# Performance work log

Measured on AMD Instinct MI355X. Metric: run time of the kernel, lower is better.

The kernel has to match this reference:

```python
import jax, jax.numpy as jnp
import numpy as np

N_EMBED = 2048
N_HEAD = 2
HEAD_SIZE = N_EMBED // N_HEAD  # 1024; mask constraint requires T <= HEAD_SIZE


def setup_inputs() -> dict:
    key = jax.random.key(0)
    ks = jax.random.split(key, 9)
    B, T, C, H, D = 32, 1024, N_EMBED, N_HEAD, HEAD_SIZE
    s = 1.0 / np.sqrt(C)
    x = jax.random.normal(ks[0], (B, T, C), dtype=jnp.float32)
    # torch Linear convention: weight (out_features, in_features), y = x @ W.T + b
    Wq = jax.random.normal(ks[1], (H, D, C), dtype=jnp.float32) * s
    Wk = jax.random.normal(ks[2], (H, D, C), dtype=jnp.float32) * s
    Wv = jax.random.normal(ks[3], (H, D, C), dtype=jnp.float32) * s
    bq = jax.random.normal(ks[4], (H, D), dtype=jnp.float32) * 0.01
    bk = jax.random.normal(ks[5], (H, D), dtype=jnp.float32) * 0.01
    bv = jax.random.normal(ks[6], (H, D), dtype=jnp.float32) * 0.01
    Wo = jax.random.normal(ks[7], (C, H * D), dtype=jnp.float32) * s  # no bias
    return {"x": x, "Wq": Wq, "bq": bq, "Wk": Wk, "bk": bk, "Wv": Wv, "bv": bv, "Wo": Wo}


def reference(x, Wq, bq, Wk, bk, Wv, bv, Wo):
    B, T, C = x.shape
    # per-head projections, batched over heads: (B,T,C) x (H,D,C) -> (B,H,T,D)
    q = jnp.einsum('btc,hdc->bhtd', x, Wq) + bq[None, :, None, :]
    k = jnp.einsum('btc,hdc->bhtd', x, Wk) + bk[None, :, None, :]
    v = jnp.einsum('btc,hdc->bhtd', x, Wv) + bv[None, :, None, :]
    # NOTE: original scales by x.shape[-1]**-0.5 == n_embed**-0.5 (not head_size)
    scale = jnp.asarray(C, x.dtype) ** -0.5
    wei = jnp.einsum('bhtd,bhsd->bhts', q, k) * scale  # (B,H,T,T)
    causal = jnp.tril(jnp.ones((T, T), dtype=bool))
    wei = jnp.where(causal[None, None], wei, -jnp.inf)
    wei = jax.nn.softmax(wei, axis=-1)
    out = jnp.einsum('bhts,bhsd->bhtd', wei, v)  # (B,H,T,D)
    # concat heads along last dim: (B,T,H*D)
    out = out.transpose(0, 2, 1, 3).reshape(B, T, -1)
    return out @ Wo.T  # (B,T,C)
```

## Files before the change

kernel.cpp:

```cpp
#include <hip/hip_runtime.h>
#include <hip/hip_bf16.h>
#include <stdint.h>

typedef __bf16 bf16_t;
typedef __bf16 bf16x8 __attribute__((ext_vector_type(8)));
typedef float f32x4 __attribute__((ext_vector_type(4)));

#define AS1(p) ((const __attribute__((address_space(1))) void*)(uintptr_t)(p))
#define AS3(p) ((__attribute__((address_space(3))) void*)(uintptr_t)(p))

__device__ __forceinline__ void gload16(const bf16_t* g, bf16_t* l) {
  __builtin_amdgcn_global_load_lds(AS1(g), AS3(l), 16, 0, 0);
}

#define BAR()    { __builtin_amdgcn_s_barrier(); __builtin_amdgcn_sched_barrier(0); }
#define VMCNT0() { asm volatile("s_waitcnt vmcnt(0)" ::: "memory"); __builtin_amdgcn_sched_barrier(0); }
#define LGKM0()  { asm volatile("s_waitcnt lgkmcnt(0)" ::: "memory"); __builtin_amdgcn_sched_barrier(0); }

__device__ __forceinline__ void gemm256(const bf16_t* __restrict__ A, int lda,
                                        const bf16_t* __restrict__ B, int ldb,
                                        int nt, f32x4 acc[8][4], bf16_t* lds) {
  const int t = (int)threadIdx.x;
  const int lane = t & 63, w = t >> 6;
  const int wr = w >> 2, wc = w & 3;
  const int fr = lane & 15, fq = lane >> 4;
  char* ldsb = (char*)lds;

  const int o = t * 16;
  const int s = o ^ (((t >> 3) & 7) << 4);
  const int r0 = s >> 6, q0 = (s >> 4) & 3;
  const bf16_t* gA0 = A + (size_t)r0 * lda + q0 * 8;
  const bf16_t* gA1 = gA0 + (size_t)128 * lda;
  const bf16_t* gB0 = B + (size_t)r0 * ldb + q0 * 8;
  const bf16_t* gB1 = gB0 + (size_t)128 * ldb;

  const int x = ((fr >> 1) & 7) << 4;
  const int abase = wr * 8192 + ((fr * 64 + fq * 16) ^ x);
  const int bbase = wc * 4096 + ((fr * 64 + fq * 16) ^ x);

  bf16x8 af[4], bvv[4];

#define STAGE_A(cb, kh, kof) \
  gload16(gA0 + (kof) + (kh) * 32, lds + (cb) * 32768 + (kh) * 8192 + t * 8); \
  gload16(gA1 + (kof) + (kh) * 32, lds + (cb) * 32768 + (kh) * 8192 + 4096 + t * 8);
#define STAGE_B(cb, kh, kof) \
  gload16(gB0 + (kof) + (kh) * 32, lds + (cb) * 32768 + 16384 + (kh) * 8192 + t * 8); \
  gload16(gB1 + (kof) + (kh) * 32, lds + (cb) * 32768 + 16384 + (kh) * 8192 + 4096 + t * 8);
#define DS_LOAD(cb, kh, qm) \
  { const char* ap = ldsb + (cb) * 65536 + (kh) * 16384 + abase + (qm) * 4096; \
    const char* bp = ldsb + (cb) * 65536 + 32768 + (kh) * 16384 + bbase; \
    _Pragma("unroll") for (int i = 0; i < 4; ++i) af[i] = *(const bf16x8*)(ap + i * 1024); \
    _Pragma("unroll") for (int n = 0; n < 4; ++n) bvv[n] = *(const bf16x8*)(bp + n * 1024); }
#define MFMA16(qm) \
  { __builtin_amdgcn_s_setprio(1); \
    _Pragma("unroll") for (int i = 0; i < 4; ++i) \
      _Pragma("unroll") for (int n = 0; n < 4; ++n) \
        acc[(qm) * 4 + i][n] = __builtin_amdgcn_mfma_f32_16x16x32_bf16(af[i], bvv[n], acc[(qm) * 4 + i][n], 0, 0, 0); \
    __builtin_amdgcn_s_setprio(0); }

  STAGE_A(0, 0, 0) STAGE_B(0, 0, 0) STAGE_A(0, 1, 0) STAGE_B(0, 1, 0)
  VMCNT0() BAR()

  int kof = 64;
  for (int tt = 0; tt < nt - 1; ++tt, kof += 64) {
    const int cb = tt & 1;
    DS_LOAD(cb, 0, 0) STAGE_A(cb ^ 1, 0, kof) STAGE_A(cb ^ 1, 1, kof) LGKM0() MFMA16(0)
    DS_LOAD(cb, 0, 1) STAGE_B(cb ^ 1, 0, kof) STAGE_B(cb ^ 1, 1, kof) LGKM0() MFMA16(1)
    DS_LOAD(cb, 1, 0) LGKM0() MFMA16(0)
    DS_LOAD(cb, 1, 1) LGKM0() MFMA16(1)
    VMCNT0() BAR()
  }
  {
    const int cb = (nt - 1) & 1;
    DS_LOAD(cb, 0, 0) LGKM0() MFMA16(0)
    DS_LOAD(cb, 0, 1) LGKM0() MFMA16(1)
    DS_LOAD(cb, 1, 0) LGKM0() MFMA16(0)
    DS_LOAD(cb, 1, 1) LGKM0() MFMA16(1)
  }
#undef STAGE_A
#undef STAGE_B
#undef DS_LOAD
#undef MFMA16
}

#define EPI_VARS \
  const int t = (int)threadIdx.x; \
  const int lane = t & 63, w = t >> 6; \
  const int wr = w >> 2, wc = w & 3; \
  const int fr = lane & 15, fq = lane >> 4;

#define ZERO8x4(acc) \
  _Pragma("unroll") for (int _i = 0; _i < 8; ++_i) \
  _Pragma("unroll") for (int _j = 0; _j < 4; ++_j) { f32x4 _z = {0.f,0.f,0.f,0.f}; acc[_i][_j] = _z; }

__global__ void k_cvt(const float* __restrict__ s, bf16_t* __restrict__ d, long n8) {
  long i = (long)blockIdx.x * blockDim.x + threadIdx.x;
  long st = (long)gridDim.x * blockDim.x;
  for (; i < n8; i += st) {
    const float4* sp = (const float4*)(s + i * 8);
    float4 a = sp[0], b = sp[1];
    bf16x8 v;
    v[0] = (__bf16)a.x; v[1] = (__bf16)a.y; v[2] = (__bf16)a.z; v[3] = (__bf16)a.w;
    v[4] = (__bf16)b.x; v[5] = (__bf16)b.y; v[6] = (__bf16)b.z; v[7] = (__bf16)b.w;
    *(bf16x8*)(d + i * 8) = v;
  }
}

__global__ void k_fill(float* o, float v, long n) {
  long i = (long)blockIdx.x * blockDim.x + threadIdx.x;
  long st = (long)gridDim.x * blockDim.x;
  for (; i < n; i += st) o[i] = v;
}

__global__ __launch_bounds__(512, 2) void k_qkv256(
    const bf16_t* __restrict__ xb, const bf16_t* __restrict__ Wb,
    const float* __restrict__ bq, const float* __restrict__ bk, const float* __restrict__ bv,
    bf16_t* __restrict__ Q, bf16_t* __restrict__ K, bf16_t* __restrict__ Vt) {
  __shared__ __align__(16) bf16_t lds[65536];
  int bid = (int)blockIdx.x;
  int id = (bid & 7) * 384 + (bid >> 3);
  EPI_VARS
  f32x4 acc[8][4];
  ZERO8x4(acc)

  bool vmode = id >= 2048;
  int mt = 0, ntile = 0, tok = 0, wm = 0;
  const bf16_t *Ap, *Bp;
  if (!vmode) {
    mt = id & 127; ntile = id >> 7;
    Ap = xb + (size_t)mt * 256 * 2048;
    Bp = Wb + (size_t)ntile * 256 * 2048;
  } else {
    int vb = id - 2048;
    tok = vb & 127; wm = vb >> 7;
    Ap = Wb + (size_t)(16 + wm) * 256 * 2048;
    Bp = xb + (size_t)tok * 256 * 2048;
  }
  gemm256(Ap, 2048, Bp, 2048, 32, acc, lds);

  if (!vmode) {
    int sel = ntile >> 3;
    const float* bias = sel ? bk : bq;
    bf16_t* dst = sel ? K : Q;
    int cbase = (ntile & 7) * 256 + wc * 64;
#pragma unroll
    for (int ni = 0; ni < 4; ++ni) {
      int c2 = cbase + ni * 16 + fr;
      int h = c2 >> 10, d = c2 & 1023;
      float bb = bias[c2];
#pragma unroll
      for (int mi = 0; mi < 8; ++mi) {
        f32x4 a = acc[mi][ni];
#pragma unroll
        for (int r = 0; r < 4; ++r) {
          int m = mt * 256 + wr * 128 + mi * 16 + fq * 4 + r;
          int b = m >> 10, tk = m & 1023;
          dst[(((size_t)(b * 2 + h) << 10) + tk) * 1024 + d] = (bf16_t)(a[r] + bb);
        }
      }
    }
  } else {
#pragma unroll
    for (int mi = 0; mi < 8; ++mi) {
#pragma unroll
      for (int r = 0; r < 4; ++r) {
        int gd = wm * 256 + wr * 128 + mi * 16 + fq * 4 + r;
        int h = gd >> 10, d = gd & 1023;
        float bb = bv[gd];
#pragma unroll
        for (int ni = 0; ni < 4; ++ni) {
          int m = tok * 256 + wc * 64 + ni * 16 + fr;
          int b = m >> 10, tk = m & 1023;
          Vt[(((size_t)(b * 2 + h) << 10) + d) * 1024 + tk] = (bf16_t)(acc[mi][ni][r] + bb);
        }
      }
    }
  }
}

__global__ __launch_bounds__(512, 2) void k_s256(const bf16_t* __restrict__ Q,
                                                 const bf16_t* __restrict__ K,
                                                 float* __restrict__ S, int pbase) {
  __shared__ __align__(16) bf16_t lds[65536];
  int id = (int)blockIdx.x;
  int pc = id / 10, rem = id % 10;
  int ti = 0;
  while (rem > ti) { rem -= ti + 1; ++ti; }
  int tj = rem;
  size_t p = (size_t)(pbase + pc);
  EPI_VARS
  f32x4 acc[8][4];
  ZERO8x4(acc)
  gemm256(Q + (p << 20) + (size_t)ti * 256 * 1024, 1024,
          K + (p << 20) + (size_t)tj * 256 * 1024, 1024, 16, acc, lds);
  float* Sp = S + ((size_t)pc << 20);
  const float scale = 0.022097086912079608f;
#pragma unroll
  for (int mi = 0; mi < 8; ++mi)
#pragma unroll
    for (int ni = 0; ni < 4; ++ni) {
      int col = tj * 256 + wc * 64 + ni * 16 + fr;
      f32x4 a = acc[mi][ni];
#pragma unroll
      for (int r = 0; r < 4; ++r) {
        int row = ti * 256 + wr * 128 + mi * 16 + fq * 4 + r;
        Sp[((size_t)row << 10) + col] = a[r] * scale;
      }
    }
}

__global__ __launch_bounds__(256) void k_softmax(const float* __restrict__ S,
                                                 bf16_t* __restrict__ P) {
  int bid = blockIdx.x;
  int pc = bid >> 10, row = bid & 1023;
  const float* s = S + ((size_t)pc << 20) + ((size_t)row << 10);
  bf16_t* p = P + ((size_t)pc << 20) + ((size_t)row << 10);
  int cend = ((row >> 8) + 1) << 8;
  int t = threadIdx.x;
  __shared__ float red[8];
  float x[4];
  float mx = -1e30f;
#pragma unroll
  for (int j = 0; j < 4; ++j) {
    int c = t + 256 * j;
    x[j] = (c <= row) ? s[c] : -1e30f;
    mx = fmaxf(mx, x[j]);
  }
  for (int o = 32; o > 0; o >>= 1) mx = fmaxf(mx, __shfl_xor(mx, o));
  if (!(t & 63)) red[t >> 6] = mx;
  __syncthreads();
  mx = fmaxf(fmaxf(red[0], red[1]), fmaxf(red[2], red[3]));
  float e[4];
  float sum = 0.f;
#pragma unroll
  for (int j = 0; j < 4; ++j) {
    e[j] = (x[j] > -1e29f) ? __expf(x[j] - mx) : 0.f;
    sum += e[j];
  }
  for (int o = 32; o > 0; o >>= 1) sum += __shfl_xor(sum, o);
  if (!(t & 63)) red[4 + (t >> 6)] = sum;
  __syncthreads();
  sum = red[4] + red[5] + red[6] + red[7];
  float inv = 1.f / sum;
#pragma unroll
  for (int j = 0; j < 4; ++j) {
    int c = t + 256 * j;
    if (c < cend) p[c] = (bf16_t)(e[j] * inv);
  }
}

__global__ __launch_bounds__(512, 2) void k_pv256(const bf16_t* __restrict__ P,
                                                  const bf16_t* __restrict__ Vt,
                                                  bf16_t* __restrict__ O, int pbase) {
  __shared__ __align__(16) bf16_t lds[65536];
  int id = (int)blockIdx.x;
  int pc = id >> 4, rem = id & 15;
  int ti = rem >> 2, dj = rem & 3;
  size_t p = (size_t)(pbase + pc);
  EPI_VARS
  f32x4 acc[8][4];
  ZERO8x4(acc)
  gemm256(P + ((size_t)pc << 20) + (size_t)ti * 256 * 1024, 1024,
          Vt + (p << 20) + (size_t)dj * 256 * 1024, 1024, (ti + 1) * 4, acc, lds);
  int b = (int)(p >> 1), h = (int)(p & 1);
#pragma unroll
  for (int mi = 0; mi < 8; ++mi)
#pragma unroll
    for (int ni = 0; ni < 4; ++ni) {
      int dcol = dj * 256 + wc * 64 + ni * 16 + fr;
      f32x4 a = acc[mi][ni];
#pragma unroll
      for (int r = 0; r < 4; ++r) {
        int tk = ti * 256 + wr * 128 + mi * 16 + fq * 4 + r;
        O[(((size_t)b << 10) + tk) * 2048 + (h << 10) + dcol] = (bf16_t)a[r];
      }
    }
}

__global__ __launch_bounds__(512, 2) void k_out256(const bf16_t* __restrict__ O,
                                                   const bf16_t* __restrict__ W,
                                                   float* __restrict__ out) {
  __shared__ __align__(16) bf16_t lds[65536];
  int bid = (int)blockIdx.x;
  int id = (bid & 7) * 128 + (bid >> 3);
  int mt = id & 127, ntile = id >> 7;
  EPI_VARS
  f32x4 acc[8][4];
  ZERO8x4(acc)
  gemm256(O + (size_t)mt * 256 * 2048, 2048, W + (size_t)ntile * 256 * 2048, 2048, 32, acc, lds);
#pragma unroll
  for (int mi = 0; mi < 8; ++mi)
#pragma unroll
    for (int ni = 0; ni < 4; ++ni) {
      int col = ntile * 256 + wc * 64 + ni * 16 + fr;
      f32x4 a = acc[mi][ni];
#pragma unroll
      for (int r = 0; r < 4; ++r) {
        int row = mt * 256 + wr * 128 + mi * 16 + fq * 4 + r;
        out[(size_t)row * 2048 + col] = a[r];
      }
    }
}

extern "C" void kernel_launch(void* const* d_in, const int* in_sizes, int n_in,
                              void* d_out, int out_size, void* d_ws, size_t ws_size,
                              hipStream_t stream) {
  const float* x  = (const float*)d_in[0];
  const float* Wq = (const float*)d_in[1];
  const float* bq = (const float*)d_in[2];
  const float* Wk = (const float*)d_in[3];
  const float* bk = (const float*)d_in[4];
  const float* Wv = (const float*)d_in[5];
  const float* bv = (const float*)d_in[6];
  const float* Wo = (const float*)d_in[7];
  float* out = (float*)d_out;

  const size_t MiB = 1ull << 20;
  char* w = (char*)d_ws;
  bf16_t* xb    = (bf16_t*)w;
  bf16_t* Ob    = xb;
  bf16_t* Qb    = (bf16_t*)(w + 128 * MiB);
  bf16_t* Kb    = (bf16_t*)(w + 256 * MiB);
  bf16_t* Vt    = (bf16_t*)(w + 384 * MiB);
  bf16_t* Wqkvb = (bf16_t*)(w + 512 * MiB);
  bf16_t* Wob   = (bf16_t*)(w + 536 * MiB);
  float*  Sc    = (float*)(w + 544 * MiB);

  size_t rem = ws_size > 544 * MiB ? ws_size - 544 * MiB : 0;
  int NP = (int)(rem / (6 * MiB));
  if (NP > 64) NP = 64;
  if (NP < 1) {
    k_fill<<<2048, 256, 0, stream>>>(out, (float)(ws_size >> 20), (long)out_size);
    return;
  }
  bf16_t* Pc = (bf16_t*)(w + 544 * MiB + (size_t)NP * 4 * MiB);

  k_cvt<<<2048, 256, 0, stream>>>(x, xb, 8388608L);
  k_cvt<<<1024, 256, 0, stream>>>(Wq, Wqkvb, 524288L);
  k_cvt<<<1024, 256, 0, stream>>>(Wk, Wqkvb + 4194304, 524288L);
  k_cvt<<<1024, 256, 0, stream>>>(Wv, Wqkvb + 8388608, 524288L);
  k_cvt<<<1024, 256, 0, stream>>>(Wo, Wob, 524288L);

  k_qkv256<<<3072, 512, 0, stream>>>(xb, Wqkvb, bq, bk, bv, Qb, Kb, Vt);

  for (int base = 0; base < 64; base += NP) {
    int np = (64 - base) < NP ? (64 - base) : NP;
    k_s256<<<np * 10, 512, 0, stream>>>(Qb, Kb, Sc, base);
    k_softmax<<<np * 1024, 256, 0, stream>>>(Sc, Pc);
    k_pv256<<<np * 16, 512, 0, stream>>>(Pc, Vt, Ob, base);
  }

  k_out256<<<1024, 512, 0, stream>>>(Ob, Wob, out);
}
```

Before: 1.515 ms.

## Restructure GEMM pipeline with partial waits, store scores in bf16, wave-per-row softmax

The shared GEMM main loop now interleaves LDS reads and global-to-LDS staging per k-half, using partial vmcnt/lgkmcnt waits and two A-fragment register sets so MFMAs overlap outstanding loads. The score matrix is written in bf16 instead of fp32, halving score traffic and letting more head-pairs fit per chunk. Softmax becomes one wavefront per row with vectorized 16-byte loads and stores, removing the shared-memory reductions and block barriers. The changes lower score precision before softmax and rely on the finer-grained wait counts being correct.

New measurement: 1.475 ms. 2.6% less time.

```diff
diff --git a/kernel.cpp b/kernel.cpp
--- a/kernel.cpp
+++ b/kernel.cpp
@@ -13,9 +13,10 @@
   __builtin_amdgcn_global_load_lds(AS1(g), AS3(l), 16, 0, 0);
 }
 
-#define BAR()    { __builtin_amdgcn_s_barrier(); __builtin_amdgcn_sched_barrier(0); }
-#define VMCNT0() { asm volatile("s_waitcnt vmcnt(0)" ::: "memory"); __builtin_amdgcn_sched_barrier(0); }
-#define LGKM0()  { asm volatile("s_waitcnt lgkmcnt(0)" ::: "memory"); __builtin_amdgcn_sched_barrier(0); }
+#define SB()      __builtin_amdgcn_sched_barrier(0);
+#define BAR()     { __builtin_amdgcn_sched_barrier(0); __builtin_amdgcn_s_barrier(); __builtin_amdgcn_sched_barrier(0); }
+#define VMCNT(n)  { asm volatile("s_waitcnt vmcnt(" #n ")" ::: "memory"); __builtin_amdgcn_sched_barrier(0); }
+#define LGKM(n)   { asm volatile("s_waitcnt lgkmcnt(" #n ")" ::: "memory"); __builtin_amdgcn_sched_barrier(0); }
 
 __device__ __forceinline__ void gemm256(const bf16_t* __restrict__ A, int lda,
                                         const bf16_t* __restrict__ B, int ldb,
@@ -26,60 +27,77 @@
   const int fr = lane & 15, fq = lane >> 4;
   char* ldsb = (char*)lds;
 
-  const int o = t * 16;
-  const int s = o ^ (((t >> 3) & 7) << 4);
-  const int r0 = s >> 6, q0 = (s >> 4) & 3;
+  const int s0 = (t * 16) ^ (((t >> 3) & 7) << 4);
+  const int r0 = s0 >> 6, q0 = (s0 >> 4) & 3;
   const bf16_t* gA0 = A + (size_t)r0 * lda + q0 * 8;
   const bf16_t* gA1 = gA0 + (size_t)128 * lda;
   const bf16_t* gB0 = B + (size_t)r0 * ldb + q0 * 8;
   const bf16_t* gB1 = gB0 + (size_t)128 * ldb;
 
-  const int x = ((fr >> 1) & 7) << 4;
-  const int abase = wr * 8192 + ((fr * 64 + fq * 16) ^ x);
-  const int bbase = wc * 4096 + ((fr * 64 + fq * 16) ^ x);
-
-  bf16x8 af[4], bvv[4];
-
-#define STAGE_A(cb, kh, kof) \
-  gload16(gA0 + (kof) + (kh) * 32, lds + (cb) * 32768 + (kh) * 8192 + t * 8); \
-  gload16(gA1 + (kof) + (kh) * 32, lds + (cb) * 32768 + (kh) * 8192 + 4096 + t * 8);
-#define STAGE_B(cb, kh, kof) \
-  gload16(gB0 + (kof) + (kh) * 32, lds + (cb) * 32768 + 16384 + (kh) * 8192 + t * 8); \
-  gload16(gB1 + (kof) + (kh) * 32, lds + (cb) * 32768 + 16384 + (kh) * 8192 + 4096 + t * 8);
-#define DS_LOAD(cb, kh, qm) \
-  { const char* ap = ldsb + (cb) * 65536 + (kh) * 16384 + abase + (qm) * 4096; \
-    const char* bp = ldsb + (cb) * 65536 + 32768 + (kh) * 16384 + bbase; \
-    _Pragma("unroll") for (int i = 0; i < 4; ++i) af[i] = *(const bf16x8*)(ap + i * 1024); \
-    _Pragma("unroll") for (int n = 0; n < 4; ++n) bvv[n] = *(const bf16x8*)(bp + n * 1024); }
-#define MFMA16(qm) \
-  { __builtin_amdgcn_s_setprio(1); \
+  const int swz = (fr * 64 + fq * 16) ^ (((fr >> 1) & 7) << 4);
+  const int abase = wr * 8192 + swz;
+  const int bbase = 32768 + wc * 4096 + swz;
+
+  bf16x8 bb[4], aa0[4], aa1[4];
+
+#define STAGE_A(cb, kh, kof) { \
+    bf16_t* _d = lds + (cb) * 32768 + (kh) * 8192; \
+    gload16(gA0 + (kof) + (kh) * 32, _d + t * 8); \
+    gload16(gA1 + (kof) + (kh) * 32, _d + 4096 + t * 8); \
+  } SB()
+#define STAGE_B(cb, kh, kof) { \
+    bf16_t* _d = lds + (cb) * 32768 + 16384 + (kh) * 8192; \
+    gload16(gB0 + (kof) + (kh) * 32, _d + t * 8); \
+    gload16(gB1 + (kof) + (kh) * 32, _d + 4096 + t * 8); \
+  } SB()
+#define READ_B(cb, kh) { \
+    const char* _b = ldsb + (cb) * 65536 + (kh) * 16384 + bbase; \
+    _Pragma("unroll") for (int n = 0; n < 4; ++n) bb[n] = *(const bf16x8*)(_b + n * 1024); }
+#define READ_A(cb, kh, qm, dst) { \
+    const char* _a = ldsb + (cb) * 65536 + (kh) * 16384 + abase + (qm) * 4096; \
+    _Pragma("unroll") for (int i = 0; i < 4; ++i) dst[i] = *(const bf16x8*)(_a + i * 1024); }
+#define MFMA16(dst, qm) { \
+    __builtin_amdgcn_s_setprio(1); \
     _Pragma("unroll") for (int i = 0; i < 4; ++i) \
       _Pragma("unroll") for (int n = 0; n < 4; ++n) \
-        acc[(qm) * 4 + i][n] = __builtin_amdgcn_mfma_f32_16x16x32_bf16(af[i], bvv[n], acc[(qm) * 4 + i][n], 0, 0, 0); \
+        acc[(qm) * 4 + i][n] = __builtin_amdgcn_mfma_f32_16x16x32_bf16(dst[i], bb[n], acc[(qm) * 4 + i][n], 0, 0, 0); \
     __builtin_amdgcn_s_setprio(0); }
 
   STAGE_A(0, 0, 0) STAGE_B(0, 0, 0) STAGE_A(0, 1, 0) STAGE_B(0, 1, 0)
-  VMCNT0() BAR()
 
   int kof = 64;
   for (int tt = 0; tt < nt - 1; ++tt, kof += 64) {
     const int cb = tt & 1;
-    DS_LOAD(cb, 0, 0) STAGE_A(cb ^ 1, 0, kof) STAGE_A(cb ^ 1, 1, kof) LGKM0() MFMA16(0)
-    DS_LOAD(cb, 0, 1) STAGE_B(cb ^ 1, 0, kof) STAGE_B(cb ^ 1, 1, kof) LGKM0() MFMA16(1)
-    DS_LOAD(cb, 1, 0) LGKM0() MFMA16(0)
-    DS_LOAD(cb, 1, 1) LGKM0() MFMA16(1)
-    VMCNT0() BAR()
+    VMCNT(4) BAR()
+    READ_B(cb, 0) READ_A(cb, 0, 0, aa0)
+    STAGE_A(cb ^ 1, 0, kof)
+    READ_A(cb, 0, 1, aa1)
+    STAGE_B(cb ^ 1, 0, kof)
+    LGKM(4) MFMA16(aa0, 0)
+    LGKM(0) MFMA16(aa1, 1)
+    VMCNT(4) BAR()
+    READ_B(cb, 1) READ_A(cb, 1, 0, aa0)
+    STAGE_A(cb ^ 1, 1, kof)
+    READ_A(cb, 1, 1, aa1)
+    STAGE_B(cb ^ 1, 1, kof)
+    LGKM(4) MFMA16(aa0, 0)
+    LGKM(0) MFMA16(aa1, 1)
   }
   {
     const int cb = (nt - 1) & 1;
-    DS_LOAD(cb, 0, 0) LGKM0() MFMA16(0)
-    DS_LOAD(cb, 0, 1) LGKM0() MFMA16(1)
-    DS_LOAD(cb, 1, 0) LGKM0() MFMA16(0)
-    DS_LOAD(cb, 1, 1) LGKM0() MFMA16(1)
+    VMCNT(4) BAR()
+    READ_B(cb, 0) READ_A(cb, 0, 0, aa0) READ_A(cb, 0, 1, aa1)
+    LGKM(4) MFMA16(aa0, 0)
+    LGKM(0) MFMA16(aa1, 1)
+    VMCNT(0) BAR()
+    READ_B(cb, 1) READ_A(cb, 1, 0, aa0) READ_A(cb, 1, 1, aa1)
+    LGKM(4) MFMA16(aa0, 0)
+    LGKM(0) MFMA16(aa1, 1)
   }
 #undef STAGE_A
 #undef STAGE_B
-#undef DS_LOAD
+#undef READ_B
+#undef READ_A
 #undef MFMA16
 }
 
@@ -165,13 +183,13 @@
 #pragma unroll
       for (int r = 0; r < 4; ++r) {
         int gd = wm * 256 + wr * 128 + mi * 16 + fq * 4 + r;
-        int h = gd >> 10, d = gd & 1023;
+        int h = gd >> 10, dd = gd & 1023;
         float bb = bv[gd];
 #pragma unroll
         for (int ni = 0; ni < 4; ++ni) {
           int m = tok * 256 + wc * 64 + ni * 16 + fr;
           int b = m >> 10, tk = m & 1023;
-          Vt[(((size_t)(b * 2 + h) << 10) + d) * 1024 + tk] = (bf16_t)(acc[mi][ni][r] + bb);
+          Vt[(((size_t)(b * 2 + h) << 10) + dd) * 1024 + tk] = (bf16_t)(acc[mi][ni][r] + bb);
         }
       }
     }
@@ -180,7 +198,7 @@
 
 __global__ __launch_bounds__(512, 2) void k_s256(const bf16_t* __restrict__ Q,
                                                  const bf16_t* __restrict__ K,
-                                                 float* __restrict__ S, int pbase) {
+                                                 bf16_t* __restrict__ S, int pbase) {
   __shared__ __align__(16) bf16_t lds[65536];
   int id = (int)blockIdx.x;
   int pc = id / 10, rem = id % 10;
@@ -193,7 +211,7 @@
   ZERO8x4(acc)
   gemm256(Q + (p << 20) + (size_t)ti * 256 * 1024, 1024,
           K + (p << 20) + (size_t)tj * 256 * 1024, 1024, 16, acc, lds);
-  float* Sp = S + ((size_t)pc << 20);
+  bf16_t* Sp = S + ((size_t)pc << 20);
   const float scale = 0.022097086912079608f;
 #pragma unroll
   for (int mi = 0; mi < 8; ++mi)
@@ -204,49 +222,47 @@
 #pragma unroll
       for (int r = 0; r < 4; ++r) {
         int row = ti * 256 + wr * 128 + mi * 16 + fq * 4 + r;
-        Sp[((size_t)row << 10) + col] = a[r] * scale;
-      }
-    }
-}
-
-__global__ __launch_bounds__(256) void k_softmax(const float* __restrict__ S,
+        Sp[((size_t)row << 10) + col] = (bf16_t)(a[r] * scale);
+      }
+    }
+}
+
+__global__ __launch_bounds__(256) void k_softmax(const bf16_t* __restrict__ S,
                                                  bf16_t* __restrict__ P) {
-  int bid = blockIdx.x;
-  int pc = bid >> 10, row = bid & 1023;
-  const float* s = S + ((size_t)pc << 20) + ((size_t)row << 10);
+  int gw = (int)blockIdx.x * 4 + ((int)threadIdx.x >> 6);
+  int pc = gw >> 10, row = gw & 1023;
+  int lane = (int)threadIdx.x & 63;
+  const bf16_t* s = S + ((size_t)pc << 20) + ((size_t)row << 10);
   bf16_t* p = P + ((size_t)pc << 20) + ((size_t)row << 10);
   int cend = ((row >> 8) + 1) << 8;
-  int t = threadIdx.x;
-  __shared__ float red[8];
-  float x[4];
+  bf16x8 v0 = *(const bf16x8*)(s + lane * 8);
+  bf16x8 v1 = *(const bf16x8*)(s + 512 + lane * 8);
+  float x[16];
   float mx = -1e30f;
 #pragma unroll
-  for (int j = 0; j < 4; ++j) {
-    int c = t + 256 * j;
-    x[j] = (c <= row) ? s[c] : -1e30f;
-    mx = fmaxf(mx, x[j]);
+  for (int j = 0; j < 8; ++j) {
+    int c0 = lane * 8 + j, c1 = 512 + lane * 8 + j;
+    x[j]     = (c0 <= row) ? (float)v0[j] : -1e30f;
+    x[8 + j] = (c1 <= row) ? (float)v1[j] : -1e30f;
+    mx = fmaxf(mx, fmaxf(x[j], x[8 + j]));
   }
   for (int o = 32; o > 0; o >>= 1) mx = fmaxf(mx, __shfl_xor(mx, o));
-  if (!(t & 63)) red[t >> 6] = mx;
-  __syncthreads();
-  mx = fmaxf(fmaxf(red[0], red[1]), fmaxf(red[2], red[3]));
-  float e[4];
   float sum = 0.f;
 #pragma unroll
-  for (int j = 0; j < 4; ++j) {
-    e[j] = (x[j] > -1e29f) ? __expf(x[j] - mx) : 0.f;
-    sum += e[j];
+  for (int j = 0; j < 16; ++j) {
+    x[j] = (x[j] > -1e29f) ? __expf(x[j] - mx) : 0.f;
+    sum += x[j];
   }
   for (int o = 32; o > 0; o >>= 1) sum += __shfl_xor(sum, o);
-  if (!(t & 63)) red[4 + (t >> 6)] = sum;
-  __syncthreads();
-  sum = red[4] + red[5] + red[6] + red[7];
   float inv = 1.f / sum;
-#pragma unroll
-  for (int j = 0; j < 4; ++j) {
-    int c = t + 256 * j;
-    if (c < cend) p[c] = (bf16_t)(e[j] * inv);
-  }
+  bf16x8 o0, o1;
+#pragma unroll
+  for (int j = 0; j < 8; ++j) {
+    o0[j] = (bf16_t)(x[j] * inv);
+    o1[j] = (bf16_t)(x[8 + j] * inv);
+  }
+  if (lane * 8 < cend)       *(bf16x8*)(p + lane * 8) = o0;
+  if (512 + lane * 8 < cend) *(bf16x8*)(p + 512 + lane * 8) = o1;
 }
 
 __global__ __launch_bounds__(512, 2) void k_pv256(const bf16_t* __restrict__ P,
@@ -324,16 +340,16 @@
   bf16_t* Vt    = (bf16_t*)(w + 384 * MiB);
   bf16_t* Wqkvb = (bf16_t*)(w + 512 * MiB);
   bf16_t* Wob   = (bf16_t*)(w + 536 * MiB);
-  float*  Sc    = (float*)(w + 544 * MiB);
+  bf16_t* Sc    = (bf16_t*)(w + 544 * MiB);
 
   size_t rem = ws_size > 544 * MiB ? ws_size - 544 * MiB : 0;
-  int NP = (int)(rem / (6 * MiB));
+  int NP = (int)(rem / (4 * MiB));
   if (NP > 64) NP = 64;
   if (NP < 1) {
     k_fill<<<2048, 256, 0, stream>>>(out, (float)(ws_size >> 20), (long)out_size);
     return;
   }
-  bf16_t* Pc = (bf16_t*)(w + 544 * MiB + (size_t)NP * 4 * MiB);
+  bf16_t* Pc = (bf16_t*)(w + 544 * MiB + (size_t)NP * 2 * MiB);
 
   k_cvt<<<2048, 256, 0, stream>>>(x, xb, 8388608L);
   k_cvt<<<1024, 256, 0, stream>>>(Wq, Wqkvb, 524288L);
@@ -346,7 +362,7 @@
   for (int base = 0; base < 64; base += NP) {
     int np = (64 - base) < NP ? (64 - base) : NP;
     k_s256<<<np * 10, 512, 0, stream>>>(Qb, Kb, Sc, base);
-    k_softmax<<<np * 1024, 256, 0, stream>>>(Sc, Pc);
+    k_softmax<<<np * 256, 256, 0, stream>>>(Sc, Pc);
     k_pv256<<<np * 16, 512, 0, stream>>>(Pc, Vt, Ob, base);
   }
 
```
